# Performance work log

Hardware: AMD Instinct MI355X
Metric: run time of the kernel (lower is better)

## Reference

```python
import jax, jax.numpy as jnp
import numpy as np

NUM_HEADS = 16
NUM_KV_HEADS = 4
HEAD_DIM = 128
LAYER_IDX = 5
MASK_VALUE = -65504.0  # torch.finfo(torch.float16).min


def setup_inputs() -> dict:
    key = jax.random.key(0)
    ks = jax.random.split(key, 7)
    B, S, H = 2, 2048, 2048
    hidden_states = jax.random.normal(ks[0], (B, S, H), dtype=jnp.float32)
    k = jax.random.normal(ks[1], (B, NUM_KV_HEADS, S, HEAD_DIM), dtype=jnp.float32)
    v = jax.random.normal(ks[2], (B, NUM_KV_HEADS, S, HEAD_DIM), dtype=jnp.float32)
    std = 0.02
    w_q = jax.random.normal(ks[3], (H, H), dtype=jnp.float32) * std
    b_q = jnp.zeros((H,), dtype=jnp.float32)
    w_proj = jax.random.normal(ks[4], (H, H), dtype=jnp.float32) * (std / np.sqrt(2 * 24))
    b_proj = jnp.zeros((H,), dtype=jnp.float32)
    return {"hidden_states": hidden_states, "key": k, "value": v,
            "w_q": w_q, "b_q": b_q, "w_proj": w_proj, "b_proj": b_proj}


def reference(hidden_states, key, value, w_q, b_q, w_proj, b_proj):
    B, S, H = hidden_states.shape
    G = NUM_HEADS // NUM_KV_HEADS  # query heads per kv head
    dtype = hidden_states.dtype

    # query projection -> [B, kv_heads, group, S, head_dim]
    q = hidden_states @ w_q.T + b_q
    q = q.reshape(B, S, NUM_KV_HEADS, G, HEAD_DIM).transpose(0, 2, 3, 1, 4)

    # bigcode-style fp32 softmax with layer-wise unscale
    unscale = float(LAYER_IDX + 1)  # scale_attention_softmax_in_fp32 and upcast
    scale_factor = (1.0 / unscale) * (HEAD_DIM ** -0.5)  # scale_attn_weights

    # scores: [B, kv_heads, group, S_q, S_k]
    scores = jnp.einsum('bkgsd,bktd->bkgst', q, key) * scale_factor

    causal = jnp.tril(jnp.ones((S, S), dtype=bool))  # [S_q, S_k]
    scores = jnp.where(causal, scores, jnp.asarray(MASK_VALUE, dtype=scores.dtype))

    probs = jax.nn.softmax((scores * unscale).astype(jnp.float32), axis=-1).astype(dtype)

    out = jnp.einsum('bkgst,bktd->bkgsd', probs, value)
    out = out.transpose(0, 3, 1, 2, 4).reshape(B, S, H)
    out = out @ w_proj.T + b_proj
    return out
```

## Files before the change

### kernel.cpp

```cpp
#include <hip/hip_runtime.h>
#include <math.h>


#define RSQ128 0.08838834764831845
#define LOG2E  1.4426950408889634
#define RS2L   ((float)(RSQ128 * LOG2E))
#define CAP2   24.0f

typedef __attribute__((ext_vector_type(8))) short short8;
typedef __attribute__((ext_vector_type(4))) float f32x4;
typedef __attribute__((ext_vector_type(16))) float f32x16;

static __device__ __forceinline__ unsigned short f2bf(float x) {
    union { float f; unsigned u; } v; v.f = x;
    unsigned r = v.u + 0x7FFFu + ((v.u >> 16) & 1u);
    return (unsigned short)(r >> 16);
}

static __device__ __forceinline__ unsigned pack_bf16(float lo, float hi) {
#if __has_builtin(__builtin_amdgcn_cvt_pk_bf16_f32)
    return __builtin_bit_cast(unsigned, __builtin_amdgcn_cvt_pk_bf16_f32(lo, hi));
#else
    return (unsigned)f2bf(lo) | ((unsigned)f2bf(hi) << 16);
#endif
}

static __device__ __forceinline__ float fexp2(float x) {
#if __has_builtin(__builtin_amdgcn_exp2f)
    return __builtin_amdgcn_exp2f(x);
#else
    return exp2f(x);
#endif
}

static __device__ __forceinline__ void gl_lds16(const void* g, void* l) {
    __builtin_amdgcn_global_load_lds(
        (const __attribute__((address_space(1))) void*)g,
        (__attribute__((address_space(3))) void*)l, 16, 0, 0);
}

static __device__ __forceinline__ void cvt8(const float* __restrict__ in,
                                            unsigned short* __restrict__ out,
                                            int i) {
    const float4 a = *(const float4*)(in + i);
    const float4 b = *(const float4*)(in + i + 4);
    short8 o;
    o[0] = (short)f2bf(a.x); o[1] = (short)f2bf(a.y);
    o[2] = (short)f2bf(a.z); o[3] = (short)f2bf(a.w);
    o[4] = (short)f2bf(b.x); o[5] = (short)f2bf(b.y);
    o[6] = (short)f2bf(b.z); o[7] = (short)f2bf(b.w);
    *(short8*)(out + i) = o;
}

__global__ void prep_all(const float* __restrict__ hs, unsigned short* __restrict__ hsb,
                         const float* __restrict__ wq, unsigned short* __restrict__ wqb,
                         const float* __restrict__ K,  unsigned short* __restrict__ Kpk,
                         const float* __restrict__ V,  unsigned short* __restrict__ Vpk)
{
    __shared__ float Ts[32][132];
    const int bid = blockIdx.x, tid = threadIdx.x;

    if (bid < 4096) {
        cvt8(hs, hsb, (bid * 256 + tid) * 8);
        return;
    }
    if (bid < 6144) {
        cvt8(wq, wqb, ((bid - 4096) * 256 + tid) * 8);
        return;
    }
    if (bid < 6656) {
        const int idx = bid - 6144;
        const int t = idx & 63, bkh = idx >> 6;
        const float* src = K + ((size_t)bkh * 2048 + t * 32) * 128;
        unsigned short* dst = Kpk + ((size_t)bkh * 64 + t) * 4096;
#pragma unroll
        for (int p = 0; p < 2; ++p) {
            const int g = p * 256 + tid;
            const int ch = g >> 5, key = g & 31;
            const float4 a = *(const float4*)(src + key * 128 + ch * 8);
            const float4 b = *(const float4*)(src + key * 128 + ch * 8 + 4);
            short8 o;
            o[0] = (short)f2bf(a.x); o[1] = (short)f2bf(a.y);
            o[2] = (short)f2bf(a.z); o[3] = (short)f2bf(a.w);
            o[4] = (short)f2bf(b.x); o[5] = (short)f2bf(b.y);
            o[6] = (short)f2bf(b.z); o[7] = (short)f2bf(b.w);
            *(short8*)(dst + ch * 256 + key * 8) = o;
        }
        return;
    }
    {
        const int idx = bid - 6656;
        const int t = idx & 63, bkh = idx >> 6;
        const float* src = V + ((size_t)bkh * 2048 + t * 32) * 128;
        unsigned short* dst = Vpk + ((size_t)bkh * 64 + t) * 4096;
#pragma unroll
        for (int p = 0; p < 4; ++p) {
            const int g = p * 256 + tid;
            const int key = g >> 5, cq = g & 31;
            const float4 v = *(const float4*)(src + key * 128 + cq * 4);
            *(float4*)&Ts[key][cq * 4] = v;
        }
        __syncthreads();
#pragma unroll
        for (int p = 0; p < 2; ++p) {
            const int g = p * 256 + tid;
            const int kc = g >> 7, d = g & 127;
            short8 o;
#pragma unroll
            for (int j = 0; j < 8; ++j) o[j] = (short)f2bf(Ts[kc * 8 + j][d]);
            *(short8*)(dst + kc * 1024 + d * 8) = o;
        }
    }
}

template <int OMODE>
__global__ __launch_bounds__(512, 2) void gemm_nt_sk(
    const unsigned short* __restrict__ A,
    const unsigned short* __restrict__ W,
    const float* __restrict__ bias,
    void* __restrict__ Cout, int M, int N, int K, float oscale)
{
    __shared__ __align__(16) unsigned short SMEM[32768];
    unsigned short* Asb = SMEM;
    unsigned short* Wsb = SMEM + 16384;

    const int tid = threadIdx.x;
    const int g = tid >> 8;
    const int t2 = tid & 255;
    const int lane = tid & 63;
    const int wq = (tid >> 6) & 3;
    const int wm = wq & 1, wn = wq >> 1;
    const int m0 = blockIdx.y * 128, n0 = blockIdx.x * 128;
    const int r0 = t2 >> 2, c0 = t2 & 3;
    const int Kh = K >> 1;

    const unsigned short* Ag = A + (size_t)(m0 + r0) * K + g * Kh + c0 * 8;
    const unsigned short* Wg = W + (size_t)(n0 + r0) * K + g * Kh + c0 * 8;

    f32x4 acc[4][4];
#pragma unroll
    for (int i = 0; i < 4; ++i)
#pragma unroll
        for (int j = 0; j < 4; ++j) acc[i][j] = (f32x4){0.f, 0.f, 0.f, 0.f};

    const int lm = lane & 15, lk = (lane >> 4) * 8;
    unsigned short* As0 = Asb + g * 8192;
    unsigned short* Ws0 = Wsb + g * 8192;

    gl_lds16(Ag,                  As0 + t2 * 8);
    gl_lds16(Ag + (size_t)64 * K, As0 + (t2 + 256) * 8);
    gl_lds16(Wg,                  Ws0 + t2 * 8);
    gl_lds16(Wg + (size_t)64 * K, Ws0 + (t2 + 256) * 8);

    int buf = 0;
    for (int k0 = 0; k0 < Kh; k0 += 32) {
        __syncthreads();
        const int kn = k0 + 32;
        if (kn < Kh) {
            unsigned short* Ad = As0 + (buf ^ 1) * 4096;
            unsigned short* Wd = Ws0 + (buf ^ 1) * 4096;
            gl_lds16(Ag + kn,                  Ad + t2 * 8);
            gl_lds16(Ag + (size_t)64 * K + kn, Ad + (t2 + 256) * 8);
            gl_lds16(Wg + kn,                  Wd + t2 * 8);
            gl_lds16(Wg + (size_t)64 * K + kn, Wd + (t2 + 256) * 8);
        }

        const unsigned short* Ar = As0 + buf * 4096;
        const unsigned short* Wr = Ws0 + buf * 4096;
        short8 a[4], b[4];
#pragma unroll
        for (int i = 0; i < 4; ++i)
            a[i] = *(const short8*)&Ar[(64 * wm + 16 * i + lm) * 32 + lk];
#pragma unroll
        for (int j = 0; j < 4; ++j)
            b[j] = *(const short8*)&Wr[(64 * wn + 16 * j + lm) * 32 + lk];
#pragma unroll
        for (int i = 0; i < 4; ++i)
#pragma unroll
            for (int j = 0; j < 4; ++j)
                acc[i][j] = __builtin_amdgcn_mfma_f32_16x16x32_bf16(a[i], b[j], acc[i][j], 0, 0, 0);
        buf ^= 1;
    }

    float* MRG = (float*)SMEM;
    __syncthreads();
    if (g == 0) {
#pragma unroll
        for (int ii = 0; ii < 2; ++ii)
#pragma unroll
            for (int j = 0; j < 4; ++j) {
                float4 v4;
                v4.x = acc[2 + ii][j][0]; v4.y = acc[2 + ii][j][1];
                v4.z = acc[2 + ii][j][2]; v4.w = acc[2 + ii][j][3];
                *(float4*)&MRG[((ii * 4 + j) * 256 + wq * 64 + lane) * 4] = v4;
            }
    } else {
#pragma unroll
        for (int ii = 0; ii < 2; ++ii)
#pragma unroll
            for (int j = 0; j < 4; ++j) {
                float4 v4;
                v4.x = acc[ii][j][0]; v4.y = acc[ii][j][1];
                v4.z = acc[ii][j][2]; v4.w = acc[ii][j][3];
                *(float4*)&MRG[8192 + ((ii * 4 + j) * 256 + wq * 64 + lane) * 4] = v4;
            }
    }
    __syncthreads();
    {
        float bv[4];
#pragma unroll
        for (int j = 0; j < 4; ++j) bv[j] = bias[n0 + 64 * wn + 16 * j + lm];
        if (g == 0) {
#pragma unroll
            for (int ii = 0; ii < 2; ++ii)
#pragma unroll
                for (int j = 0; j < 4; ++j) {
                    const float4 v4 = *(const float4*)&MRG[8192 + ((ii * 4 + j) * 256 + wq * 64 + lane) * 4];
                    const float s[4] = {v4.x, v4.y, v4.z, v4.w};
#pragma unroll
                    for (int reg = 0; reg < 4; ++reg) {
                        const int row = m0 + 64 * wm + 16 * ii + 4 * (lane >> 4) + reg;
                        const int col = n0 + 64 * wn + 16 * j + lm;
                        const float v = (acc[ii][j][reg] + s[reg] + bv[j]) * oscale;
                        if (OMODE == 0) {
                            ((float*)Cout)[(size_t)row * N + col] = v;
                        } else {
                            const int bb = row >> 11, ss = row & 2047;
                            const int hh = col >> 7, dd = col & 127;
                            const size_t o = (size_t)((bb * 16 + hh) * 64 + (ss >> 5)) * 4096
                                           + (dd >> 3) * 256 + (ss & 31) * 8 + (dd & 7);
                            ((unsigned short*)Cout)[o] = f2bf(v);
                        }
                    }
                }
        } else {
#pragma unroll
            for (int ii = 0; ii < 2; ++ii)
#pragma unroll
                for (int j = 0; j < 4; ++j) {
                    const float4 v4 = *(const float4*)&MRG[((ii * 4 + j) * 256 + wq * 64 + lane) * 4];
                    const float s[4] = {v4.x, v4.y, v4.z, v4.w};
#pragma unroll
                    for (int reg = 0; reg < 4; ++reg) {
                        const int row = m0 + 64 * wm + 16 * (2 + ii) + 4 * (lane >> 4) + reg;
                        const int col = n0 + 64 * wn + 16 * j + lm;
                        const float v = (acc[2 + ii][j][reg] + s[reg] + bv[j]) * oscale;
                        if (OMODE == 0) {
                            ((float*)Cout)[(size_t)row * N + col] = v;
                        } else {
                            const int bb = row >> 11, ss = row & 2047;
                            const int hh = col >> 7, dd = col & 127;
                            const size_t o = (size_t)((bb * 16 + hh) * 64 + (ss >> 5)) * 4096
                                           + (dd >> 3) * 256 + (ss & 31) * 8 + (dd & 7);
                            ((unsigned short*)Cout)[o] = f2bf(v);
                        }
                    }
                }
        }
    }
}

__global__ __launch_bounds__(128, 3) void attn_mfma12(
    const unsigned short* __restrict__ Qpk,
    const unsigned short* __restrict__ Kpk,
    const unsigned short* __restrict__ Vpk,
    unsigned short* __restrict__ O,
    const float* __restrict__ wp,
    unsigned short* __restrict__ wpb)
{
    __shared__ __align__(16) float MRG[4096];
    __shared__ float Lsm[64];

    const int tid = threadIdx.x;

    if (blockIdx.x >= 2048) {
        const int i = ((blockIdx.x - 2048) * 128 + tid) * 8;
        cvt8(wp, wpb, i);
        return;
    }

    const int lane = tid & 63, pz = tid >> 6;
    const int h2 = lane >> 5, ln = lane & 31;

    const int bid = blockIdx.x;
    const int grp = bid & 7;
    const int idx = bid >> 3;
    const int b = grp >> 2, kh = grp & 3;
    const int hl = idx & 3;
    const int qt = 63 - (idx >> 2);
    const int h = kh * 4 + hl;

    const unsigned short* Kbase = Kpk + (size_t)(b * 4 + kh) * 64 * 4096;
    const unsigned short* Vbase = Vpk + (size_t)(b * 4 + kh) * 64 * 4096;
    const int koff = h2 * 256 + ln * 8;
    const int voff = h2 * 1024 + ln * 8;

    unsigned short* QL = (unsigned short*)MRG;
    {
        const unsigned short* qsrc = Qpk + (size_t)((b * 16 + h) * 64 + qt) * 4096;
#pragma unroll
        for (int i = 0; i < 4; ++i)
            gl_lds16(qsrc + (i * 128 + tid) * 8, QL + (i * 128 + pz * 64) * 8);
    }

    f32x16 Ot[4];
#pragma unroll
    for (int mt = 0; mt < 4; ++mt)
#pragma unroll
        for (int r = 0; r < 16; ++r) Ot[mt][r] = 0.f;
    float l_ = 0.f;

    __syncthreads();

    const int q_lo = qt * 32;
    const int qg = q_lo + ln;
    const int q_hi = q_lo + 31;
    const int jmax = qt >> 1;

    for (int j = 0; j <= jmax; ++j) {
        const int t0 = 64 * j + 32 * pz;
        if (t0 > q_hi) continue;

        const unsigned short* Kt = Kbase + (size_t)(2 * j + pz) * 4096;
        const unsigned short* Vt = Vbase + (size_t)(2 * j + pz) * 4096;

        short8 kf[8], vf[8];
#pragma unroll
        for (int ks = 0; ks < 8; ++ks)
            kf[ks] = *(const short8*)(Kt + ks * 512 + koff);
#pragma unroll
        for (int i = 0; i < 8; ++i)
            vf[i] = *(const short8*)(Vt + (i >> 2) * 2048 + (i & 3) * 256 + voff);

        f32x16 St;
#pragma unroll
        for (int r = 0; r < 16; ++r) St[r] = 0.f;
#pragma unroll
        for (int ks = 0; ks < 8; ++ks) {
            const short8 qf = *(const short8*)(QL + ks * 512 + h2 * 256 + ln * 8);
            St = __builtin_amdgcn_mfma_f32_32x32x16_bf16(kf[ks], qf, St, 0, 0, 0);
        }

        float s_loc = 0.f;
        unsigned Pp[8];
        if (t0 + 31 <= q_lo) {
#pragma unroll
            for (int p = 0; p < 8; ++p) {
                const float p0 = fexp2(St[2 * p] - CAP2);
                const float p1 = fexp2(St[2 * p + 1] - CAP2);
                s_loc += p0 + p1;
                Pp[p] = pack_bf16(p0, p1);
            }
        } else {
#pragma unroll
            for (int p = 0; p < 8; ++p) {
                const int k0 = t0 + (2 * p & 3) + 8 * (2 * p >> 2) + 4 * h2;
                const int k1 = t0 + ((2 * p + 1) & 3) + 8 * ((2 * p + 1) >> 2) + 4 * h2;
                const float p0 = (k0 <= qg) ? fexp2(St[2 * p] - CAP2) : 0.f;
                const float p1 = (k1 <= qg) ? fexp2(St[2 * p + 1] - CAP2) : 0.f;
                s_loc += p0 + p1;
                Pp[p] = pack_bf16(p0, p1);
            }
        }
        s_loc += __shfl_xor(s_loc, 32);
        l_ += s_loc;

#pragma unroll
        for (int ks4 = 0; ks4 < 2; ++ks4) {
            const unsigned pa = Pp[4 * ks4 + 0], pb = Pp[4 * ks4 + 1];
            const unsigned pc = Pp[4 * ks4 + 2], pd = Pp[4 * ks4 + 3];
            const unsigned x0 = (unsigned)__shfl_xor((int)(h2 ? pa : pc), 32);
            const unsigned x1 = (unsigned)__shfl_xor((int)(h2 ? pb : pd), 32);
            union { unsigned u[4]; short8 s8; } fr;
            fr.u[0] = h2 ? x0 : pa;
            fr.u[1] = h2 ? x1 : pb;
            fr.u[2] = h2 ? pc : x0;
            fr.u[3] = h2 ? pd : x1;
#pragma unroll
            for (int mt = 0; mt < 4; ++mt)
                Ot[mt] = __builtin_amdgcn_mfma_f32_32x32x16_bf16(vf[ks4 * 4 + mt], fr.s8, Ot[mt], 0, 0, 0);
        }
    }

    __syncthreads();
    if (pz == 1) {
#pragma unroll
        for (int mt = 0; mt < 4; ++mt)
#pragma unroll
            for (int g = 0; g < 4; ++g) {
                float4 v4;
                v4.x = Ot[mt][4 * g + 0]; v4.y = Ot[mt][4 * g + 1];
                v4.z = Ot[mt][4 * g + 2]; v4.w = Ot[mt][4 * g + 3];
                *(float4*)&MRG[lane * 64 + (((mt * 4 + g + lane) & 15) * 4)] = v4;
            }
        Lsm[lane] = l_;
    }
    __syncthreads();
    if (pz == 0) {
        l_ += Lsm[lane];
#pragma unroll
        for (int mt = 0; mt < 4; ++mt)
#pragma unroll
            for (int g = 0; g < 4; ++g) {
                const float4 v4 = *(const float4*)&MRG[lane * 64 + (((mt * 4 + g + lane) & 15) * 4)];
                Ot[mt][4 * g + 0] += v4.x;
                Ot[mt][4 * g + 1] += v4.y;
                Ot[mt][4 * g + 2] += v4.z;
                Ot[mt][4 * g + 3] += v4.w;
            }
    }
    __syncthreads();

    if (pz == 0) {
        unsigned short* Es = (unsigned short*)MRG;
        const float inv = 1.0f / l_;
#pragma unroll
        for (int mt = 0; mt < 4; ++mt)
#pragma unroll
            for (int g = 0; g < 4; ++g) {
                uint2 pk;
                pk.x = pack_bf16(Ot[mt][4 * g + 0] * inv, Ot[mt][4 * g + 1] * inv);
                pk.y = pack_bf16(Ot[mt][4 * g + 2] * inv, Ot[mt][4 * g + 3] * inv);
                const int chunk = (4 * mt + g) ^ (ln & 15);
                *(uint2*)&Es[ln * 128 + chunk * 8 + 4 * h2] = pk;
            }
    }
    __syncthreads();
    if (pz == 0) {
        unsigned short* Es = (unsigned short*)MRG;
#pragma unroll
        for (int pp = 0; pp < 8; ++pp) {
            const int f = pp * 64 + lane;
            const int q = f >> 4, c = f & 15;
            const short8 v = *(const short8*)&Es[q * 128 + ((c ^ (q & 15)) * 8)];
            *(short8*)(O + (size_t)(b * 2048 + q_lo + q) * 2048 + h * 128 + c * 8) = v;
        }
    }
}

extern "C" void kernel_launch(void* const* d_in, const int* in_sizes, int n_in,
                              void* d_out, int out_size, void* d_ws, size_t ws_size,
                              hipStream_t stream) {
    const float* hs = (const float*)d_in[0];
    const float* k  = (const float*)d_in[1];
    const float* v  = (const float*)d_in[2];
    const float* wq = (const float*)d_in[3];
    const float* bq = (const float*)d_in[4];
    const float* wp = (const float*)d_in[5];
    const float* bp = (const float*)d_in[6];
    float* out = (float*)d_out;

    unsigned short* hsb  = (unsigned short*)d_ws;
    unsigned short* wqb  = hsb  + 8388608;
    unsigned short* kpk  = wqb  + 4194304;
    unsigned short* vpk  = kpk  + 2097152;
    unsigned short* qbuf = vpk  + 2097152;
    unsigned short* abuf = qbuf + 8388608;
    unsigned short* wpb  = hsb;

    prep_all<<<7168, 256, 0, stream>>>(hs, hsb, wq, wqb, k, kpk, v, vpk);

    dim3 gG(16, 32);
    gemm_nt_sk<2><<<gG, 512, 0, stream>>>(hsb, wqb, bq, qbuf, 4096, 2048, 2048, RS2L);
    attn_mfma12<<<6144, 128, 0, stream>>>(qbuf, kpk, vpk, abuf, wp, wpb);
    gemm_nt_sk<0><<<gG, 512, 0, stream>>>(abuf, wpb, bp, out, 4096, 2048, 2048, 1.0f);
}
```

Measured before the change: 264.6 us.

## Move K/V bf16 packing from prep kernel into extra blocks of Q-projection GEMM

The K and V conversion and repacking work is removed from the prep kernel and appended as 512 extra blocks (grid y 32..63) of the Q-projection GEMM launch. Those blocks convert K and V tiles with 512 threads and return early. The aim is to shorten the memory-bound prep phase and let the K/V packing overlap with GEMM compute on otherwise idle CUs. The cost is a larger GEMM grid, and the packing blocks may be scheduled after the GEMM tiles, which could lengthen the GEMM's tail.

Measured after the change: 264.7 us. No clear change (+0.0%).

```diff
diff --git a/kernel.cpp b/kernel.cpp
--- a/kernel.cpp
+++ b/kernel.cpp
@@ -53,30 +53,36 @@
 }
 
 __global__ void prep_all(const float* __restrict__ hs, unsigned short* __restrict__ hsb,
-                         const float* __restrict__ wq, unsigned short* __restrict__ wqb,
-                         const float* __restrict__ K,  unsigned short* __restrict__ Kpk,
-                         const float* __restrict__ V,  unsigned short* __restrict__ Vpk)
+                         const float* __restrict__ wq, unsigned short* __restrict__ wqb)
 {
-    __shared__ float Ts[32][132];
     const int bid = blockIdx.x, tid = threadIdx.x;
-
     if (bid < 4096) {
         cvt8(hs, hsb, (bid * 256 + tid) * 8);
         return;
     }
-    if (bid < 6144) {
-        cvt8(wq, wqb, ((bid - 4096) * 256 + tid) * 8);
-        return;
-    }
-    if (bid < 6656) {
-        const int idx = bid - 6144;
-        const int t = idx & 63, bkh = idx >> 6;
-        const float* src = K + ((size_t)bkh * 2048 + t * 32) * 128;
-        unsigned short* dst = Kpk + ((size_t)bkh * 64 + t) * 4096;
-#pragma unroll
-        for (int p = 0; p < 2; ++p) {
-            const int g = p * 256 + tid;
-            const int ch = g >> 5, key = g & 31;
+    cvt8(wq, wqb, ((bid - 4096) * 256 + tid) * 8);
+}
+
+template <int OMODE, bool PREP>
+__global__ __launch_bounds__(512, 2) void gemm_nt_sk(
+    const unsigned short* __restrict__ A,
+    const unsigned short* __restrict__ W,
+    const float* __restrict__ bias,
+    void* __restrict__ Cout, int M, int N, int K, float oscale,
+    const float* __restrict__ Kin, const float* __restrict__ Vin,
+    unsigned short* __restrict__ Kpk, unsigned short* __restrict__ Vpk)
+{
+    __shared__ __align__(16) unsigned short SMEM[32768];
+
+    const int tid = threadIdx.x;
+
+    if (PREP && blockIdx.y >= 32) {
+        const int job = (blockIdx.y - 32) * 16 + blockIdx.x;
+        const int t = job & 63, bkh = job >> 6;
+        {
+            const float* src = Kin + ((size_t)bkh * 2048 + t * 32) * 128;
+            unsigned short* dst = Kpk + ((size_t)bkh * 64 + t) * 4096;
+            const int ch = tid >> 5, key = tid & 31;
             const float4 a = *(const float4*)(src + key * 128 + ch * 8);
             const float4 b = *(const float4*)(src + key * 128 + ch * 8 + 4);
             short8 o;
@@ -86,45 +92,30 @@
             o[6] = (short)f2bf(b.z); o[7] = (short)f2bf(b.w);
             *(short8*)(dst + ch * 256 + key * 8) = o;
         }
+        {
+            float* Ts = (float*)SMEM;
+            const float* src = Vin + ((size_t)bkh * 2048 + t * 32) * 128;
+            unsigned short* dst = Vpk + ((size_t)bkh * 64 + t) * 4096;
+#pragma unroll
+            for (int p = 0; p < 2; ++p) {
+                const int g = p * 512 + tid;
+                const int key = g >> 5, cq = g & 31;
+                const float4 v = *(const float4*)(src + key * 128 + cq * 4);
+                *(float4*)&Ts[key * 132 + cq * 4] = v;
+            }
+            __syncthreads();
+            const int kc = tid >> 7, d = tid & 127;
+            short8 o;
+#pragma unroll
+            for (int j = 0; j < 8; ++j) o[j] = (short)f2bf(Ts[(kc * 8 + j) * 132 + d]);
+            *(short8*)(dst + kc * 1024 + d * 8) = o;
+        }
         return;
     }
-    {
-        const int idx = bid - 6656;
-        const int t = idx & 63, bkh = idx >> 6;
-        const float* src = V + ((size_t)bkh * 2048 + t * 32) * 128;
-        unsigned short* dst = Vpk + ((size_t)bkh * 64 + t) * 4096;
-#pragma unroll
-        for (int p = 0; p < 4; ++p) {
-            const int g = p * 256 + tid;
-            const int key = g >> 5, cq = g & 31;
-            const float4 v = *(const float4*)(src + key * 128 + cq * 4);
-            *(float4*)&Ts[key][cq * 4] = v;
-        }
-        __syncthreads();
-#pragma unroll
-        for (int p = 0; p < 2; ++p) {
-            const int g = p * 256 + tid;
-            const int kc = g >> 7, d = g & 127;
-            short8 o;
-#pragma unroll
-            for (int j = 0; j < 8; ++j) o[j] = (short)f2bf(Ts[kc * 8 + j][d]);
-            *(short8*)(dst + kc * 1024 + d * 8) = o;
-        }
-    }
-}
-
-template <int OMODE>
-__global__ __launch_bounds__(512, 2) void gemm_nt_sk(
-    const unsigned short* __restrict__ A,
-    const unsigned short* __restrict__ W,
-    const float* __restrict__ bias,
-    void* __restrict__ Cout, int M, int N, int K, float oscale)
-{
-    __shared__ __align__(16) unsigned short SMEM[32768];
+
     unsigned short* Asb = SMEM;
     unsigned short* Wsb = SMEM + 16384;
 
-    const int tid = threadIdx.x;
     const int g = tid >> 8;
     const int t2 = tid & 255;
     const int lane = tid & 63;
@@ -458,10 +449,12 @@
     unsigned short* abuf = qbuf + 8388608;
     unsigned short* wpb  = hsb;
 
-    prep_all<<<7168, 256, 0, stream>>>(hs, hsb, wq, wqb, k, kpk, v, vpk);
-
-    dim3 gG(16, 32);
-    gemm_nt_sk<2><<<gG, 512, 0, stream>>>(hsb, wqb, bq, qbuf, 4096, 2048, 2048, RS2L);
+    prep_all<<<6144, 256, 0, stream>>>(hs, hsb, wq, wqb);
+
+    gemm_nt_sk<2, true><<<dim3(16, 64), 512, 0, stream>>>(
+        hsb, wqb, bq, qbuf, 4096, 2048, 2048, RS2L, k, v, kpk, vpk);
     attn_mfma12<<<6144, 128, 0, stream>>>(qbuf, kpk, vpk, abuf, wp, wpb);
-    gemm_nt_sk<0><<<gG, 512, 0, stream>>>(abuf, wpb, bp, out, 4096, 2048, 2048, 1.0f);
-}
+    gemm_nt_sk<0, false><<<dim3(16, 32), 512, 0, stream>>>(
+        abuf, wpb, bp, out, 4096, 2048, 2048, 1.0f,
+        nullptr, nullptr, nullptr, nullptr);
+}
```
